# Optimization experiments

Measured on AMD Instinct MI355X. Metric: run time of the kernel, lower is better.

## Reference

```python
import jax, jax.numpy as jnp
import numpy as np

B, N, D = 4, 2048, 1024
H, DH = 16, 64
SCALE = DH ** -0.5


def setup_inputs() -> dict:
    key = jax.random.key(0)
    k1, k2, k3 = jax.random.split(key, 3)
    z = jax.random.normal(k1, (B, N, D), dtype=jnp.float32)
    w_qkv = jax.random.normal(k2, (D, 3 * H * DH), dtype=jnp.float32) * (D ** -0.5)
    w_out = jax.random.normal(k3, (H * DH, D), dtype=jnp.float32) * ((H * DH) ** -0.5)
    b_out = jnp.zeros((D,), dtype=jnp.float32)
    return {"z": z, "w_qkv": w_qkv, "w_out": w_out, "b_out": b_out}


def reference(z, w_qkv, w_out, b_out):
    # qkv projection: (B,N,D) @ (D,3*H*DH) -> split into q,k,v
    qkv = z @ w_qkv  # (B, N, 3*H*DH)
    q, k, v = jnp.split(qkv, 3, axis=-1)
    # (B, N, H*DH) -> (B, H, N, DH)
    def heads(t):
        return t.reshape(B, N, H, DH).transpose(0, 2, 1, 3)
    q, k, v = heads(q), heads(k), heads(v)
    # scaled dot-product attention with full NxN scores (matches original)
    dots = jnp.einsum('bhid,bhjd->bhij', q, k) * SCALE
    attn = jax.nn.softmax(dots, axis=-1)
    out = jnp.einsum('bhij,bhjd->bhid', attn, v)  # (B, H, N, DH)
    out = out.transpose(0, 2, 1, 3).reshape(B, N, H * DH)
    return out @ w_out + b_out  # dropout is identity in eval
```

## Files before the change

kernel.cpp:

```cpp
#include <hip/hip_runtime.h>
#include <hip/hip_bf16.h>
#include <cstdint>
#include <cstddef>

typedef __attribute__((ext_vector_type(8))) short short8;
typedef __attribute__((ext_vector_type(4))) float f32x4;
typedef __attribute__((ext_vector_type(4))) unsigned uint4v;

#define LDS_AS __attribute__((address_space(3)))
#define GLB_AS __attribute__((address_space(1)))

__device__ __forceinline__ unsigned short f32_bf16(float f) {
  unsigned u = __builtin_bit_cast(unsigned, f);
  u += 0x7fffu + ((u >> 16) & 1u);
  return (unsigned short)(u >> 16);
}

__device__ __forceinline__ unsigned cvt_pk_bf16(float lo, float hi) {
  unsigned r;
  asm("v_cvt_pk_bf16_f32 %0, %1, %2" : "=v"(r) : "v"(lo), "v"(hi));
  return r;
}

__global__ __launch_bounds__(256) void k_cvt(const float* __restrict__ in,
                                             unsigned short* __restrict__ out, int n4) {
  int i = blockIdx.x * 256 + threadIdx.x;
  if (i >= n4) return;
  float4 v = reinterpret_cast<const float4*>(in)[i];
  ushort4 o;
  o.x = f32_bf16(v.x); o.y = f32_bf16(v.y); o.z = f32_bf16(v.z); o.w = f32_bf16(v.w);
  reinterpret_cast<ushort4*>(out)[i] = o;
}

__global__ __launch_bounds__(256) void k_cvt_t(const float* __restrict__ in,
                                               unsigned short* __restrict__ out,
                                               int R, int C) {
  __shared__ float t[32][33];
  int c0 = blockIdx.x * 32, r0 = blockIdx.y * 32;
  int lr = threadIdx.x & 31, lw = threadIdx.x >> 5;
#pragma unroll
  for (int i = 0; i < 32; i += 8)
    t[lw + i][lr] = in[(size_t)(r0 + lw + i) * C + c0 + lr];
  __syncthreads();
#pragma unroll
  for (int i = 0; i < 32; i += 8)
    out[(size_t)(c0 + lw + i) * R + r0 + lr] = f32_bf16(t[lr][lw + i]);
}

__device__ __forceinline__ void gemm_bt_mainloop(
    const unsigned short* __restrict__ A, const unsigned short* __restrict__ Bt,
    int K, int m0, int n0, unsigned short* lds, int tid, f32x4 acc[4][4]) {
  const int w = tid >> 6, l = tid & 63;
  const int wr = w >> 1, wc = w & 1;
  const int lr = l & 15, lg = l >> 4;
  unsigned short* As = lds;
  unsigned short* Bs = lds + 8192;
  const int sslot = tid & 7;
  for (int kt = 0; kt < K; kt += 64) {
    __syncthreads();
#pragma unroll
    for (int i = 0; i < 4; ++i) {
      int idx = i * 256 + tid;
      int row = idx >> 3;
      int sw = sslot ^ (row & 7);
      __builtin_amdgcn_global_load_lds(
          (const GLB_AS unsigned int*)(A + (size_t)(m0 + row) * K + kt + sw * 8),
          (LDS_AS unsigned int*)(As + (size_t)idx * 8), 16, 0, 0);
    }
#pragma unroll
    for (int i = 0; i < 4; ++i) {
      int idx = i * 256 + tid;
      int row = idx >> 3;
      int sw = sslot ^ (row & 7);
      __builtin_amdgcn_global_load_lds(
          (const GLB_AS unsigned int*)(Bt + (size_t)(n0 + row) * K + kt + sw * 8),
          (LDS_AS unsigned int*)(Bs + (size_t)idx * 8), 16, 0, 0);
    }
    __syncthreads();
#pragma unroll
    for (int kc = 0; kc < 2; ++kc) {
      const int so = ((kc * 4 + lg) ^ (lr & 7)) * 8;
      short8 a[4], b[4];
#pragma unroll
      for (int m = 0; m < 4; ++m)
        a[m] = *reinterpret_cast<const short8*>(As + (wr * 64 + m * 16 + lr) * 64 + so);
#pragma unroll
      for (int n = 0; n < 4; ++n)
        b[n] = *reinterpret_cast<const short8*>(Bs + (wc * 64 + n * 16 + lr) * 64 + so);
      __builtin_amdgcn_s_setprio(1);
#pragma unroll
      for (int m = 0; m < 4; ++m)
#pragma unroll
        for (int n = 0; n < 4; ++n)
          acc[m][n] = __builtin_amdgcn_mfma_f32_16x16x32_bf16(a[m], b[n], acc[m][n], 0, 0, 0);
      __builtin_amdgcn_s_setprio(0);
    }
  }
}

__global__ __launch_bounds__(256) void k_gemm_qkv(
    const unsigned short* __restrict__ Zb, const unsigned short* __restrict__ Wt,
    unsigned short* __restrict__ Qb, unsigned short* __restrict__ Kb,
    unsigned short* __restrict__ Vt) {
  __shared__ unsigned short lds[16384];
  f32x4 acc[4][4];
#pragma unroll
  for (int m = 0; m < 4; ++m)
#pragma unroll
    for (int n = 0; n < 4; ++n) acc[m][n] = (f32x4){0.f, 0.f, 0.f, 0.f};
  const int m0 = blockIdx.x * 128, n0 = blockIdx.y * 128;
  gemm_bt_mainloop(Zb, Wt, 1024, m0, n0, lds, threadIdx.x, acc);
  const int tid = threadIdx.x, w = tid >> 6, l = tid & 63;
  const int wr = w >> 1, wc = w & 1, lr = l & 15, lg = l >> 4;
#pragma unroll
  for (int n = 0; n < 4; ++n) {
    int gc = n0 + wc * 64 + n * 16;
    int part = gc >> 10;
    int within = gc & 1023;
    int h = within >> 6;
    int dhb = (within & 63) + lr;
#pragma unroll
    for (int m = 0; m < 4; ++m) {
      int gr = m0 + wr * 64 + m * 16 + lg * 4;
      int b = gr >> 11, pos = gr & 2047;
      size_t bh = (size_t)(b * 16 + h);
      if (part == 0) {
        unsigned short* dst = Qb + bh * (2048 * 64) + (size_t)pos * 64 + dhb;
#pragma unroll
        for (int r = 0; r < 4; ++r) dst[r * 64] = f32_bf16(acc[m][n][r]);
      } else if (part == 1) {
        unsigned short* dst = Kb + bh * (2048 * 64) + (size_t)pos * 64 + dhb;
#pragma unroll
        for (int r = 0; r < 4; ++r) dst[r * 64] = f32_bf16(acc[m][n][r]);
      } else {
        unsigned short* dst = Vt + bh * (64 * 2048) + (size_t)dhb * 2048 + pos;
        ushort4 pv;
        pv.x = f32_bf16(acc[m][n][0]); pv.y = f32_bf16(acc[m][n][1]);
        pv.z = f32_bf16(acc[m][n][2]); pv.w = f32_bf16(acc[m][n][3]);
        *reinterpret_cast<ushort4*>(dst) = pv;
      }
    }
  }
}

__device__ __forceinline__ void softmax_pack(f32x4 s[4], float& m_r, float& l_r,
                                             f32x4 o[4], short8 pb[2], bool lgodd,
                                             float cc) {
  float t0 = fmaxf(fmaxf(s[0][0], s[0][1]), s[0][2]);
  float t1 = fmaxf(fmaxf(s[0][3], s[1][0]), s[1][1]);
  float t2 = fmaxf(fmaxf(s[1][2], s[1][3]), s[2][0]);
  float t3 = fmaxf(fmaxf(s[2][1], s[2][2]), s[2][3]);
  float t4 = fmaxf(fmaxf(s[3][0], s[3][1]), s[3][2]);
  float tl = fmaxf(fmaxf(fmaxf(t0, t1), fmaxf(t2, t3)), fmaxf(t4, s[3][3]));
  if (__any(tl > m_r + 8.0f)) {
    float tm = fmaxf(tl, __shfl_xor(tl, 16));
    tm = fmaxf(tm, __shfl_xor(tm, 32));
    float mn = fmaxf(m_r, tm);
    float al = __builtin_amdgcn_exp2f((m_r - mn) * cc);
    m_r = mn;
    l_r *= al;
#pragma unroll
    for (int c = 0; c < 4; ++c)
#pragma unroll
      for (int r = 0; r < 4; ++r) o[c][r] *= al;
  }
  float nb = m_r * cc;
  float rs = 0.f;
#pragma unroll
  for (int c = 0; c < 4; ++c)
#pragma unroll
    for (int r = 0; r < 4; ++r) {
      float p = __builtin_amdgcn_exp2f(s[c][r] * cc - nb);
      s[c][r] = p;
      rs += p;
    }
  rs += __shfl_xor(rs, 16);
  rs += __shfl_xor(rs, 32);
  l_r += rs;
  unsigned Ap[4], Bp[4];
#pragma unroll
  for (int c = 0; c < 4; ++c) {
    Ap[c] = cvt_pk_bf16(s[c][0], s[c][1]);
    Bp[c] = cvt_pk_bf16(s[c][2], s[c][3]);
  }
#pragma unroll
  for (int kc = 0; kc < 2; ++kc) {
    unsigned ua = Ap[2 * kc], va = Ap[2 * kc + 1];
    asm("v_permlane32_swap_b32 %0, %1" : "+v"(ua), "+v"(va));
    unsigned uas = (unsigned)__shfl_xor((int)ua, 16);
    unsigned vas = (unsigned)__shfl_xor((int)va, 16);
    unsigned w0 = lgodd ? vas : ua;
    unsigned w2 = lgodd ? va : uas;
    unsigned ub = Bp[2 * kc], vb = Bp[2 * kc + 1];
    asm("v_permlane32_swap_b32 %0, %1" : "+v"(ub), "+v"(vb));
    unsigned ubs = (unsigned)__shfl_xor((int)ub, 16);
    unsigned vbs = (unsigned)__shfl_xor((int)vb, 16);
    unsigned w1 = lgodd ? vbs : ub;
    unsigned w3 = lgodd ? vb : ubs;
    uint4v pw = (uint4v){w0, w1, w2, w3};
    pb[kc] = __builtin_bit_cast(short8, pw);
  }
}

__global__ __launch_bounds__(256, 4) void k_attn(
    const unsigned short* __restrict__ Q, const unsigned short* __restrict__ Kb,
    const unsigned short* __restrict__ Vt, unsigned short* __restrict__ O) {
  __shared__ unsigned short lds[16384];
  const int tid = threadIdx.x, w = tid >> 6, l = tid & 63;
  const int lr = l & 15, lg = l >> 4;
  const bool lgodd = (lg & 1) != 0;
  const int wg = blockIdx.x;
  const int xcd = wg & 7, local = wg >> 3;
  const int bh = xcd + ((local >> 4) << 3);
  const int qb = local & 15;
  const unsigned short* Qp = Q + (size_t)bh * (2048 * 64);
  const unsigned short* Kp = Kb + (size_t)bh * (2048 * 64);
  const unsigned short* Vp = Vt + (size_t)bh * (64 * 2048);
  const int q0 = qb * 128 + w * 32;

  short8 aq[2][2];
#pragma unroll
  for (int g = 0; g < 2; ++g)
#pragma unroll
    for (int kc = 0; kc < 2; ++kc)
      aq[g][kc] = *reinterpret_cast<const short8*>(
          Qp + (size_t)(q0 + g * 16 + lr) * 64 + kc * 32 + lg * 8);

  float m0r = -3e38f, l0r = 0.f, m1r = -3e38f, l1r = 0.f;
  f32x4 o0[4], o1[4];
#pragma unroll
  for (int c = 0; c < 4; ++c) {
    o0[c] = (f32x4){0.f, 0.f, 0.f, 0.f};
    o1[c] = (f32x4){0.f, 0.f, 0.f, 0.f};
  }
  const f32x4 zero4 = (f32x4){0.f, 0.f, 0.f, 0.f};
  const float cc = 0.125f * 1.44269504089f;

  const int so0 = (lg ^ (lr & 7)) * 8;
  const int so1 = ((4 + lg) ^ (lr & 7)) * 8;

  const int srow = tid >> 3, sslot = tid & 7;
#define STAGE_KV(bufK, bufV, kv0)                                                     \
  {                                                                                   \
    _Pragma("unroll")                                                                 \
    for (int i = 0; i < 2; ++i) {                                                     \
      int row = i * 32 + srow;                                                        \
      int sw = sslot ^ (row & 7);                                                     \
      __builtin_amdgcn_global_load_lds(                                               \
          (const GLB_AS unsigned int*)(Kp + (size_t)((kv0) + row) * 64 + sw * 8),     \
          (LDS_AS unsigned int*)((bufK) + (i * 256 + tid) * 8), 16, 0, 0);            \
      __builtin_amdgcn_global_load_lds(                                               \
          (const GLB_AS unsigned int*)(Vp + (size_t)row * 2048 + (kv0) + sw * 8),     \
          (LDS_AS unsigned int*)((bufV) + (i * 256 + tid) * 8), 16, 0, 0);            \
    }                                                                                 \
  }

  unsigned short* K0 = lds;
  unsigned short* V0 = lds + 4096;
  unsigned short* K1 = lds + 8192;
  unsigned short* V1 = lds + 12288;

  STAGE_KV(K0, V0, 0);
  __syncthreads();

  for (int t = 0; t < 32; ++t) {
    unsigned short* Ks = (t & 1) ? K1 : K0;
    unsigned short* Vs = (t & 1) ? V1 : V0;
    if (t < 31) {
      unsigned short* Kn = (t & 1) ? K0 : K1;
      unsigned short* Vn = (t & 1) ? V0 : V1;
      STAGE_KV(Kn, Vn, (t + 1) * 64);
    }
    f32x4 s0[4], s1[4];
    __builtin_amdgcn_s_setprio(1);
#pragma unroll
    for (int c = 0; c < 4; ++c) {
      const unsigned short* kb = Ks + c * 1024 + lr * 64;
      short8 ak0 = *reinterpret_cast<const short8*>(kb + so0);
      short8 ak1 = *reinterpret_cast<const short8*>(kb + so1);
      s0[c] = __builtin_amdgcn_mfma_f32_16x16x32_bf16(ak0, aq[0][0], zero4, 0, 0, 0);
      s1[c] = __builtin_amdgcn_mfma_f32_16x16x32_bf16(ak0, aq[1][0], zero4, 0, 0, 0);
      s0[c] = __builtin_amdgcn_mfma_f32_16x16x32_bf16(ak1, aq[0][1], s0[c], 0, 0, 0);
      s1[c] = __builtin_amdgcn_mfma_f32_16x16x32_bf16(ak1, aq[1][1], s1[c], 0, 0, 0);
    }
    __builtin_amdgcn_s_setprio(0);
    short8 pb0[2], pb1[2];
    softmax_pack(s0, m0r, l0r, o0, pb0, lgodd, cc);
    softmax_pack(s1, m1r, l1r, o1, pb1, lgodd, cc);
    __builtin_amdgcn_s_setprio(1);
#pragma unroll
    for (int c = 0; c < 4; ++c) {
      const unsigned short* vb = Vs + c * 1024 + lr * 64;
      short8 av0 = *reinterpret_cast<const short8*>(vb + so0);
      short8 av1 = *reinterpret_cast<const short8*>(vb + so1);
      o0[c] = __builtin_amdgcn_mfma_f32_16x16x32_bf16(av0, pb0[0], o0[c], 0, 0, 0);
      o1[c] = __builtin_amdgcn_mfma_f32_16x16x32_bf16(av0, pb1[0], o1[c], 0, 0, 0);
      o0[c] = __builtin_amdgcn_mfma_f32_16x16x32_bf16(av1, pb0[1], o0[c], 0, 0, 0);
      o1[c] = __builtin_amdgcn_mfma_f32_16x16x32_bf16(av1, pb1[1], o1[c], 0, 0, 0);
    }
    __builtin_amdgcn_s_setprio(0);
    __syncthreads();
  }

  const int b = bh >> 4, h = bh & 15;
#pragma unroll
  for (int g = 0; g < 2; ++g) {
    const float inv = 1.0f / (g ? l1r : l0r);
    const f32x4* o = g ? o1 : o0;
    const size_t row = (size_t)b * 2048 + q0 + g * 16 + lr;
#pragma unroll
    for (int c = 0; c < 4; ++c) {
      ushort4 pv;
      pv.x = f32_bf16(o[c][0] * inv);
      pv.y = f32_bf16(o[c][1] * inv);
      pv.z = f32_bf16(o[c][2] * inv);
      pv.w = f32_bf16(o[c][3] * inv);
      *reinterpret_cast<ushort4*>(const_cast<unsigned short*>(
          O + row * 1024 + h * 64 + c * 16 + lg * 4)) = pv;
    }
  }
#undef STAGE_KV
}

__global__ __launch_bounds__(256) void k_gemm_out(
    const unsigned short* __restrict__ Ob, const unsigned short* __restrict__ Wt,
    const float* __restrict__ bias, float* __restrict__ out) {
  __shared__ unsigned short lds[16384];
  f32x4 acc[4][4];
#pragma unroll
  for (int m = 0; m < 4; ++m)
#pragma unroll
    for (int n = 0; n < 4; ++n) acc[m][n] = (f32x4){0.f, 0.f, 0.f, 0.f};
  const int m0 = blockIdx.x * 128, n0 = blockIdx.y * 128;
  gemm_bt_mainloop(Ob, Wt, 1024, m0, n0, lds, threadIdx.x, acc);
  const int tid = threadIdx.x, w = tid >> 6, l = tid & 63;
  const int wr = w >> 1, wc = w & 1, lr = l & 15, lg = l >> 4;
#pragma unroll
  for (int n = 0; n < 4; ++n) {
    int gc = n0 + wc * 64 + n * 16 + lr;
    float bo = bias[gc];
#pragma unroll
    for (int m = 0; m < 4; ++m) {
      int gr = m0 + wr * 64 + m * 16 + lg * 4;
#pragma unroll
      for (int r = 0; r < 4; ++r)
        out[(size_t)(gr + r) * 1024 + gc] = acc[m][n][r] + bo;
    }
  }
}

extern "C" void kernel_launch(void* const* d_in, const int* in_sizes, int n_in,
                              void* d_out, int out_size, void* d_ws, size_t ws_size,
                              hipStream_t stream) {
  const float* z     = (const float*)d_in[0];
  const float* w_qkv = (const float*)d_in[1];
  const float* w_out = (const float*)d_in[2];
  const float* b_out = (const float*)d_in[3];
  float* out = (float*)d_out;

  unsigned short* ws = (unsigned short*)d_ws;
  unsigned short* Zb    = ws;
  unsigned short* Wqkvt = ws + 8388608;
  unsigned short* Woutt = ws + 11534336;
  unsigned short* Qb    = ws + 12582912;
  unsigned short* Kb    = ws + 20971520;
  unsigned short* Vt    = ws + 29360128;
  unsigned short* Ob    = Zb;

  k_cvt<<<dim3(8192), dim3(256), 0, stream>>>(z, Zb, 2097152);
  k_cvt_t<<<dim3(96, 32), dim3(256), 0, stream>>>(w_qkv, Wqkvt, 1024, 3072);
  k_cvt_t<<<dim3(32, 32), dim3(256), 0, stream>>>(w_out, Woutt, 1024, 1024);
  k_gemm_qkv<<<dim3(64, 24), dim3(256), 0, stream>>>(Zb, Wqkvt, Qb, Kb, Vt);
  k_attn<<<dim3(1024), dim3(256), 0, stream>>>(Qb, Kb, Vt, Ob);
  k_gemm_out<<<dim3(64, 8), dim3(256), 0, stream>>>(Ob, Woutt, b_out, out);
}
```

Measured before the change: 203.2 us.

## Double attention block to 512 threads and merge weight transpose kernels

The attention kernel now runs 8 waves per block over 256 query rows instead of 4 waves over 128. Each K/V tile staged in LDS is therefore shared by twice as many waves, and each thread issues a single staging load per tile. The two weight convert-transpose launches are merged into one kernel that picks its source by block index, saving a launch. The larger blocks halve the grid to 512 and may lower occupancy under the 4-blocks launch bound.

```diff
diff --git a/kernel.cpp b/kernel.cpp
--- a/kernel.cpp
+++ b/kernel.cpp
@@ -32,11 +32,19 @@
   reinterpret_cast<ushort4*>(out)[i] = o;
 }
 
-__global__ __launch_bounds__(256) void k_cvt_t(const float* __restrict__ in,
-                                               unsigned short* __restrict__ out,
-                                               int R, int C) {
+__global__ __launch_bounds__(256) void k_cvt_t2(const float* __restrict__ wq,
+                                                unsigned short* __restrict__ oq,
+                                                const float* __restrict__ wo,
+                                                unsigned short* __restrict__ oo) {
   __shared__ float t[32][33];
-  int c0 = blockIdx.x * 32, r0 = blockIdx.y * 32;
+  int bx = blockIdx.x;
+  const float* in;
+  unsigned short* out;
+  int C;
+  if (bx < 96) { in = wq; out = oq; C = 3072; }
+  else         { in = wo; out = oo; C = 1024; bx -= 96; }
+  const int R = 1024;
+  int c0 = bx * 32, r0 = blockIdx.y * 32;
   int lr = threadIdx.x & 31, lw = threadIdx.x >> 5;
 #pragma unroll
   for (int i = 0; i < 32; i += 8)
@@ -202,7 +210,7 @@
   }
 }
 
-__global__ __launch_bounds__(256, 4) void k_attn(
+__global__ __launch_bounds__(512, 4) void k_attn(
     const unsigned short* __restrict__ Q, const unsigned short* __restrict__ Kb,
     const unsigned short* __restrict__ Vt, unsigned short* __restrict__ O) {
   __shared__ unsigned short lds[16384];
@@ -211,12 +219,12 @@
   const bool lgodd = (lg & 1) != 0;
   const int wg = blockIdx.x;
   const int xcd = wg & 7, local = wg >> 3;
-  const int bh = xcd + ((local >> 4) << 3);
-  const int qb = local & 15;
+  const int bh = xcd + ((local >> 3) << 3);
+  const int qb = local & 7;
   const unsigned short* Qp = Q + (size_t)bh * (2048 * 64);
   const unsigned short* Kp = Kb + (size_t)bh * (2048 * 64);
   const unsigned short* Vp = Vt + (size_t)bh * (64 * 2048);
-  const int q0 = qb * 128 + w * 32;
+  const int q0 = qb * 256 + w * 32;
 
   short8 aq[2][2];
 #pragma unroll
@@ -240,19 +248,15 @@
   const int so1 = ((4 + lg) ^ (lr & 7)) * 8;
 
   const int srow = tid >> 3, sslot = tid & 7;
+  const int ssw = sslot ^ (srow & 7);
 #define STAGE_KV(bufK, bufV, kv0)                                                     \
   {                                                                                   \
-    _Pragma("unroll")                                                                 \
-    for (int i = 0; i < 2; ++i) {                                                     \
-      int row = i * 32 + srow;                                                        \
-      int sw = sslot ^ (row & 7);                                                     \
-      __builtin_amdgcn_global_load_lds(                                               \
-          (const GLB_AS unsigned int*)(Kp + (size_t)((kv0) + row) * 64 + sw * 8),     \
-          (LDS_AS unsigned int*)((bufK) + (i * 256 + tid) * 8), 16, 0, 0);            \
-      __builtin_amdgcn_global_load_lds(                                               \
-          (const GLB_AS unsigned int*)(Vp + (size_t)row * 2048 + (kv0) + sw * 8),     \
-          (LDS_AS unsigned int*)((bufV) + (i * 256 + tid) * 8), 16, 0, 0);            \
-    }                                                                                 \
+    __builtin_amdgcn_global_load_lds(                                                 \
+        (const GLB_AS unsigned int*)(Kp + (size_t)((kv0) + srow) * 64 + ssw * 8),     \
+        (LDS_AS unsigned int*)((bufK) + tid * 8), 16, 0, 0);                          \
+    __builtin_amdgcn_global_load_lds(                                                 \
+        (const GLB_AS unsigned int*)(Vp + (size_t)srow * 2048 + (kv0) + ssw * 8),     \
+        (LDS_AS unsigned int*)((bufV) + tid * 8), 16, 0, 0);                          \
   }
 
   unsigned short* K0 = lds;
@@ -368,9 +372,8 @@
   unsigned short* Ob    = Zb;
 
   k_cvt<<<dim3(8192), dim3(256), 0, stream>>>(z, Zb, 2097152);
-  k_cvt_t<<<dim3(96, 32), dim3(256), 0, stream>>>(w_qkv, Wqkvt, 1024, 3072);
-  k_cvt_t<<<dim3(32, 32), dim3(256), 0, stream>>>(w_out, Woutt, 1024, 1024);
+  k_cvt_t2<<<dim3(128, 32), dim3(256), 0, stream>>>(w_qkv, Wqkvt, w_out, Woutt);
   k_gemm_qkv<<<dim3(64, 24), dim3(256), 0, stream>>>(Zb, Wqkvt, Qb, Kb, Vt);
-  k_attn<<<dim3(1024), dim3(256), 0, stream>>>(Qb, Kb, Vt, Ob);
+  k_attn<<<dim3(512), dim3(512), 0, stream>>>(Qb, Kb, Vt, Ob);
   k_gemm_out<<<dim3(64, 8), dim3(256), 0, stream>>>(Ob, Woutt, b_out, out);
 }
```

Measured after the change: 196.3 us. -3.4%, faster.
